# Kernel optimization log

Measured on AMD Instinct MI355X. Metric: run time of the kernel, lower is better.

Reference implementation:

```python
import jax, jax.numpy as jnp
import numpy as np

B, T, H, S, OBS, ACT = 64, 256, 1024, 128, 1024, 32


def setup_inputs() -> dict:
    key = jax.random.key(0)
    ks = jax.random.split(key, 9)
    w = lambda k, shape, fan_in: jax.random.normal(k, shape, jnp.float32) / np.sqrt(fan_in).astype(np.float32)
    return {
        "obs": jax.random.normal(ks[0], (B, T, OBS), jnp.float32),
        "action": jax.random.normal(ks[1], (B, T, ACT), jnp.float32),
        "resets": jnp.zeros((B,), jnp.bool_),
        "noise": jax.random.normal(ks[2], (B, T, S), jnp.float32),
        # GRUCell params (PyTorch layout: gates ordered r,z,n)
        "w_ih": w(ks[3], (3 * H, S + ACT), S + ACT),
        "w_hh": w(ks[4], (3 * H, H), H),
        "b_ih": jnp.zeros((3 * H,), jnp.float32),
        "b_hh": jnp.zeros((3 * H,), jnp.float32),
        # prior MLP: H -> H//2 -> 2S
        "pr_w1": w(ks[5], (H // 2, H), H),
        "pr_b1": jnp.zeros((H // 2,), jnp.float32),
        "pr_w2": w(ks[6], (2 * S, H // 2), H // 2),
        "pr_b2": jnp.zeros((2 * S,), jnp.float32),
        # posterior MLP: (H+OBS) -> (H+OBS)//2 -> 2S
        "po_w1": w(ks[7], ((H + OBS) // 2, H + OBS), H + OBS),
        "po_b1": jnp.zeros(((H + OBS) // 2,), jnp.float32),
        "po_w2": w(ks[8], (2 * S, (H + OBS) // 2), (H + OBS) // 2),
        "po_b2": jnp.zeros((2 * S,), jnp.float32),
    }


def reference(obs, action, resets, noise, w_ih, w_hh, b_ih, b_hh,
              pr_w1, pr_b1, pr_w2, pr_b2, po_w1, po_b1, po_w2, po_b2):
    Bv, Tv, _ = obs.shape
    keep = (~resets).astype(obs.dtype)[:, None]  # [B,1]; multiplies h,z for t>0
    # prev_action: zeros at t=0, action[:, t-1] afterwards
    prev_act = jnp.concatenate([jnp.zeros_like(action[:, :1]), action[:, :-1]], axis=1)

    def step(carry, xs):
        h, z = carry
        a_t, o_t, n_t, t_pos = xs
        m = jnp.where(t_pos > 0, keep, jnp.ones_like(keep))
        h = h * m
        z = z * m
        x = jnp.concatenate([z, a_t], axis=-1)
        gi = x @ w_ih.T + b_ih
        gh = h @ w_hh.T + b_hh
        ir, iz, inn = jnp.split(gi, 3, axis=-1)
        hr, hz, hn = jnp.split(gh, 3, axis=-1)
        r = jax.nn.sigmoid(ir + hr)
        u = jax.nn.sigmoid(iz + hz)
        n = jnp.tanh(inn + r * hn)
        h = (1.0 - u) * n + u * h
        pp = jax.nn.relu(h @ pr_w1.T + pr_b1) @ pr_w2.T + pr_b2
        pm, ps = jnp.split(pp, 2, axis=-1)
        ps = jax.nn.softplus(ps) + 1e-6
        qp = jax.nn.relu(jnp.concatenate([h, o_t], axis=-1) @ po_w1.T + po_b1) @ po_w2.T + po_b2
        qm, qs = jnp.split(qp, 2, axis=-1)
        qs = jax.nn.softplus(qs) + 1e-6
        z = qm + qs * n_t  # reparameterized rsample
        return (h, z), (h, z, pm, ps, qm, qs)

    h0 = jnp.zeros((Bv, w_hh.shape[-1]), obs.dtype)
    z0 = jnp.zeros((Bv, noise.shape[-1]), obs.dtype)
    xs = (jnp.swapaxes(prev_act, 0, 1), jnp.swapaxes(obs, 0, 1),
          jnp.swapaxes(noise, 0, 1), jnp.arange(Tv))
    _, (hs, zs, pm, ps, qm, qs) = jax.lax.scan(step, (h0, z0), xs)
    h_seq = jnp.swapaxes(hs, 0, 1)  # [B,T,H]
    z_seq = jnp.swapaxes(zs, 0, 1)  # [B,T,S]
    to_last = lambda a: jnp.moveaxis(a, 0, -1)  # torch stacks dists along dim=-1 -> [B,S,T]
    return (to_last(pm), to_last(ps), to_last(qm), to_last(qs), h_seq, z_seq)
```

## Files before the change

### kernel.cpp

```cpp
#include <hip/hip_runtime.h>

#define B_ 64
#define T_ 256
#define H_ 1024
#define S_ 128
#define OBS_ 1024
#define ACT_ 32

typedef __attribute__((ext_vector_type(8))) short bf16x8;
typedef __attribute__((ext_vector_type(4))) float f32x4;

#define MFMA(a, b, c) __builtin_amdgcn_mfma_f32_16x16x32_bf16((a), (b), (c), 0, 0, 0)

__device__ __forceinline__ float bf2f(short s) {
    unsigned int u = ((unsigned int)(unsigned short)s) << 16;
    float f; __builtin_memcpy(&f, &u, 4); return f;
}
__device__ __forceinline__ short f2bf(float f) {
    unsigned int u; __builtin_memcpy(&u, &f, 4);
    unsigned int r = (u + 0x7fffu + ((u >> 16) & 1u)) >> 16;
    return (short)r;
}
__device__ __forceinline__ bf16x8 ld8(const short* p) { return *(const bf16x8*)p; }
__device__ __forceinline__ bf16x8 cvt8(const float* p) {
    bf16x8 r;
#pragma unroll
    for (int i = 0; i < 8; ++i) r[i] = f2bf(p[i]);
    return r;
}
__device__ __forceinline__ bf16x8 lda8(const short* p) {
    const unsigned long long* q8 = (const unsigned long long*)p;
    union { unsigned long long q[2]; bf16x8 v; } u;
    u.q[0] = __hip_atomic_load(q8, __ATOMIC_RELAXED, __HIP_MEMORY_SCOPE_AGENT);
    u.q[1] = __hip_atomic_load(q8 + 1, __ATOMIC_RELAXED, __HIP_MEMORY_SCOPE_AGENT);
    return u.v;
}
__device__ __forceinline__ void sta8(short* p, unsigned long long v) {
    __hip_atomic_store((unsigned long long*)p, v, __ATOMIC_RELAXED, __HIP_MEMORY_SCOPE_AGENT);
}
__device__ __forceinline__ unsigned long long pk4(float4 v) {
    return (unsigned long long)(unsigned short)f2bf(v.x)
         | ((unsigned long long)(unsigned short)f2bf(v.y) << 16)
         | ((unsigned long long)(unsigned short)f2bf(v.z) << 32)
         | ((unsigned long long)(unsigned short)f2bf(v.w) << 48);
}
__device__ __forceinline__ float sigm(float x) { return 1.f / (1.f + __expf(-x)); }
__device__ __forceinline__ float tanh_f(float x) { return 1.f - 2.f / (__expf(2.f * x) + 1.f); }
__device__ __forceinline__ float splus(float x) { return (x > 20.f) ? x : log1pf(__expf(x)); }

__device__ __forceinline__ void gridbar(int* flags, int e) {
    __syncthreads();
    if (threadIdx.x == 0)
        __hip_atomic_store(&flags[blockIdx.x * 16], e, __ATOMIC_RELAXED, __HIP_MEMORY_SCOPE_AGENT);
    if (threadIdx.x < 64) {
        while (__hip_atomic_load(&flags[threadIdx.x * 16], __ATOMIC_RELAXED,
                                 __HIP_MEMORY_SCOPE_AGENT) < e)
            __builtin_amdgcn_s_sleep(1);
    }
    __syncthreads();
}

__global__ void f2bf_arr(const float* __restrict__ src, short* __restrict__ dst, int n4) {
    int i = blockIdx.x * blockDim.x + threadIdx.x;
    if (i < n4) {
        float4 v = ((const float4*)src)[i];
        short4 o;
        o.x = f2bf(v.x); o.y = f2bf(v.y); o.z = f2bf(v.z); o.w = f2bf(v.w);
        ((short4*)dst)[i] = o;
    }
}

__global__ __launch_bounds__(256) void obs_gemm(
    const float* __restrict__ obs, const short* __restrict__ po_w1,
    const float* __restrict__ po_b1, short* __restrict__ part) {
    const int t = blockIdx.x;
    const int rg = threadIdx.x >> 6, lane = threadIdx.x & 63;
    const int c = lane & 15, q = lane >> 4;
    bf16x8 afr[32];
    const float* ap = obs + ((size_t)(rg * 16 + c) * T_ + t) * OBS_;
#pragma unroll
    for (int kb = 0; kb < 32; ++kb) afr[kb] = cvt8(ap + kb * 32 + q * 8);
    for (int jt = 0; jt < 64; ++jt) {
        f32x4 acc = {0.f, 0.f, 0.f, 0.f};
        const short* wgt = po_w1 + (size_t)(jt * 16 + c) * 2048 + 1024;
#pragma unroll 8
        for (int kb = 0; kb < 32; ++kb) acc = MFMA(afr[kb], ld8(wgt + kb * 32 + q * 8), acc);
        const float bias = po_b1[jt * 16 + c];
#pragma unroll
        for (int e = 0; e < 4; ++e) {
            const int br = rg * 16 + q * 4 + e;
            part[((size_t)t * 64 + br) * 1024 + jt * 16 + c] = f2bf(acc[e] + bias);
        }
    }
}

__global__ __launch_bounds__(256, 1) void rssm_scan(
    const short* __restrict__ act_bf, const unsigned char* __restrict__ resets,
    const short* __restrict__ w_ih, const short* __restrict__ w_hh,
    const float* __restrict__ b_ih, const float* __restrict__ b_hh,
    const short* __restrict__ po_w1, const short* __restrict__ po_w2,
    const float* __restrict__ po_b2, const short* __restrict__ part,
    const float* __restrict__ noise,
    int* flags, short* h_bf, short* z_bf, short* poh,
    float* __restrict__ out_h, float* __restrict__ out_qm,
    float* __restrict__ out_qs, float* __restrict__ out_z) {
    extern __shared__ __align__(16) char smem[];
    bf16x8* wlds = (bf16x8*)smem;
    __shared__ __align__(16) float stg[64][20];
    const int tid = threadIdx.x, bid = blockIdx.x;
    const int rg = tid >> 6, lane = tid & 63, c = lane & 15, q = lane >> 4;
    const int j0 = bid * 16, m0 = rg * 16, arow = m0 + c, n = j0 + c;
    const int srow = tid >> 2, sseg = tid & 3;
    const bf16x8 zv8 = {0, 0, 0, 0, 0, 0, 0, 0};

    for (int i = 0; i < 32; ++i) {
        const int fid = i * 256 + tid;
        const int g = fid >> 11, kb = (fid >> 6) & 31, ln = fid & 63;
        const int cc = ln & 15, qq = ln >> 4;
        const short* src = (g == 0)
            ? po_w1 + (size_t)(j0 + cc) * 2048 + kb * 32 + qq * 8
            : w_hh + (size_t)((g - 1) * 1024 + j0 + cc) * 1024 + kb * 32 + qq * 8;
        wlds[fid] = ld8(src);
    }
    __syncthreads();

    const bool rsA = resets[arow] != 0;
    bool rsR[4];
#pragma unroll
    for (int e = 0; e < 4; ++e) rsR[e] = resets[m0 + q * 4 + e] != 0;
    const short* wiR = w_ih + (size_t)n * 160;
    const short* wiU = w_ih + (size_t)(1024 + n) * 160;
    const short* wiN = w_ih + (size_t)(2048 + n) * 160;
    const float biR = b_ih[n], bhR = b_hh[n];
    const float biU = b_ih[1024 + n], bhU = b_hh[1024 + n];
    const float biN = b_ih[2048 + n], bhN = b_hh[2048 + n];
    const short* ha = h_bf + arow * 1024;
    const bf16x8* wPl = wlds;
    const bf16x8* wRl = wlds + 2048;
    const bf16x8* wUl = wlds + 4096;
    const bf16x8* wNl = wlds + 6144;
    const int s2 = (bid < 8) ? j0 + c : 0;
    const short* wm = po_w2 + (size_t)s2 * 1024;
    const short* ws2 = po_w2 + (size_t)(128 + s2) * 1024;
    const float bM = (bid < 8) ? po_b2[s2] : 0.f;
    const float bS = (bid < 8) ? po_b2[128 + s2] : 0.f;

    f32x4 hp = {0.f, 0.f, 0.f, 0.f};
    f32x4 gR = {0.f, 0.f, 0.f, 0.f};
    f32x4 gU = {0.f, 0.f, 0.f, 0.f};
    f32x4 gN = {0.f, 0.f, 0.f, 0.f};
    f32x4 pinit;
#pragma unroll
    for (int e = 0; e < 4; ++e)
        pinit[e] = bf2f(part[((size_t)0 * 64 + m0 + q * 4 + e) * 1024 + n]);

    int ep = 1;
    for (int t = 0; t < T_; ++t) {
        f32x4 iR = {0.f, 0.f, 0.f, 0.f};
        f32x4 iU = iR, iN = iR;
        if (t > 0) {
            const short* za = z_bf + arow * 128;
#pragma unroll
            for (int kb = 0; kb < 4; ++kb) {
                const int k = kb * 32 + q * 8;
                bf16x8 a = rsA ? zv8 : lda8(za + k);
                iR = MFMA(a, ld8(wiR + k), iR);
                iU = MFMA(a, ld8(wiU + k), iU);
                iN = MFMA(a, ld8(wiN + k), iN);
            }
            const int k = q * 8;
            bf16x8 a2 = ld8(act_bf + (size_t)arow * (T_ * ACT_) + (size_t)(t - 1) * ACT_ + k);
            iR = MFMA(a2, ld8(wiR + 128 + k), iR);
            iU = MFMA(a2, ld8(wiU + 128 + k), iU);
            iN = MFMA(a2, ld8(wiN + 128 + k), iN);
        }
#pragma unroll
        for (int e = 0; e < 4; ++e) {
            const float hpv = (t > 0 && rsR[e]) ? 0.f : hp[e];
            const float r = sigm(iR[e] + gR[e] + biR + bhR);
            const float u = sigm(iU[e] + gU[e] + biU + bhU);
            const float nn = tanh_f(iN[e] + biN + r * (gN[e] + bhN));
            const float hv = (1.f - u) * nn + u * hpv;
            hp[e] = hv;
            stg[m0 + q * 4 + e][c] = hv;
        }
        __syncthreads();
        {
            float4 hv4 = *(const float4*)&stg[srow][sseg * 4];
            sta8(h_bf + srow * 1024 + j0 + sseg * 4, pk4(hv4));
            *(float4*)(out_h + (size_t)srow * (T_ * H_) + (size_t)t * H_ + j0 + sseg * 4) = hv4;
        }
        gridbar(flags, ep++);
        {
            f32x4 accP = pinit;
            f32x4 nR = {0.f, 0.f, 0.f, 0.f};
            f32x4 nU = nR, nN = nR;
#pragma unroll 8
            for (int kb = 0; kb < 32; ++kb) {
                const int k = kb * 32 + q * 8;
                bf16x8 a = lda8(ha + k);
                bf16x8 am = rsA ? zv8 : a;
                accP = MFMA(a, wPl[kb * 64 + lane], accP);
                nR = MFMA(am, wRl[kb * 64 + lane], nR);
                nU = MFMA(am, wUl[kb * 64 + lane], nU);
                nN = MFMA(am, wNl[kb * 64 + lane], nN);
            }
            gR = nR; gU = nU; gN = nN;
#pragma unroll
            for (int e = 0; e < 4; ++e) stg[m0 + q * 4 + e][c] = fmaxf(accP[e], 0.f);
        }
        if (t + 1 < T_) {
#pragma unroll
            for (int e = 0; e < 4; ++e)
                pinit[e] = bf2f(part[((size_t)(t + 1) * 64 + m0 + q * 4 + e) * 1024 + n]);
        }
        float nz[4];
        if (bid < 8) {
#pragma unroll
            for (int e = 0; e < 4; ++e)
                nz[e] = noise[(size_t)(m0 + q * 4 + e) * (T_ * S_) + (size_t)t * S_ + s2];
        }
        __syncthreads();
        {
            float4 v4 = *(const float4*)&stg[srow][sseg * 4];
            sta8(poh + srow * 1024 + j0 + sseg * 4, pk4(v4));
        }
        gridbar(flags, ep++);
        if (bid < 8) {
            f32x4 aM = {0.f, 0.f, 0.f, 0.f};
            f32x4 aS = aM;
            const short* pa = poh + arow * 1024;
#pragma unroll 8
            for (int kb = 0; kb < 32; ++kb) {
                const int k = kb * 32 + q * 8;
                bf16x8 a = lda8(pa + k);
                aM = MFMA(a, ld8(wm + k), aM);
                aS = MFMA(a, ld8(ws2 + k), aS);
            }
#pragma unroll
            for (int e = 0; e < 4; ++e) {
                const int row = m0 + q * 4 + e;
                const float qm = aM[e] + bM;
                const float qs = splus(aS[e] + bS) + 1e-6f;
                stg[row][c] = qm + qs * nz[e];
                out_qm[(size_t)row * (S_ * T_) + (size_t)s2 * T_ + t] = qm;
                out_qs[(size_t)row * (S_ * T_) + (size_t)s2 * T_ + t] = qs;
            }
            __syncthreads();
            {
                float4 z4 = *(const float4*)&stg[srow][sseg * 4];
                *(float4*)(out_z + (size_t)srow * (T_ * S_) + (size_t)t * S_ + j0 + sseg * 4) = z4;
                sta8(z_bf + srow * 128 + j0 + sseg * 4, pk4(z4));
            }
        }
        gridbar(flags, ep++);
    }
}

__global__ __launch_bounds__(256) void prior_mlp(
    const float* __restrict__ hseq, const short* __restrict__ pr_w1,
    const float* __restrict__ pr_b1, const short* __restrict__ pr_w2,
    const float* __restrict__ pr_b2, float* __restrict__ out_pm,
    float* __restrict__ out_ps) {
    __shared__ __align__(16) short hid[64][512];
    const int w = threadIdx.x >> 6;
    const int lane = threadIdx.x & 63;
    const int c = lane & 15, q = lane >> 4;
    const long rb0 = (long)blockIdx.x * 64;
    bf16x8 afr[32];
    const float* ap = hseq + (rb0 + w * 16 + c) * 1024;
#pragma unroll
    for (int kb = 0; kb < 32; ++kb) afr[kb] = cvt8(ap + kb * 32 + q * 8);
    for (int jt = 0; jt < 32; ++jt) {
        f32x4 acc = {0.f, 0.f, 0.f, 0.f};
        const short* wgt = pr_w1 + (size_t)(jt * 16 + c) * 1024;
#pragma unroll 8
        for (int kb = 0; kb < 32; ++kb) acc = MFMA(afr[kb], ld8(wgt + kb * 32 + q * 8), acc);
        const float bias = pr_b1[jt * 16 + c];
#pragma unroll
        for (int e = 0; e < 4; ++e)
            hid[w * 16 + q * 4 + e][jt * 16 + c] = f2bf(fmaxf(acc[e] + bias, 0.f));
    }
    __syncthreads();
    bf16x8 afr2[16];
#pragma unroll
    for (int kb = 0; kb < 16; ++kb) afr2[kb] = *(const bf16x8*)(&hid[w * 16 + c][kb * 32 + q * 8]);
    for (int jt = 0; jt < 16; ++jt) {
        f32x4 acc = {0.f, 0.f, 0.f, 0.f};
        const short* wgt = pr_w2 + (size_t)(jt * 16 + c) * 512;
#pragma unroll 8
        for (int kb = 0; kb < 16; ++kb) acc = MFMA(afr2[kb], ld8(wgt + kb * 32 + q * 8), acc);
        const int col = jt * 16 + c;
#pragma unroll
        for (int e = 0; e < 4; ++e) {
            const long rgidx = rb0 + w * 16 + q * 4 + e;
            const int b_ = (int)(rgidx >> 8), t_ = (int)(rgidx & 255);
            if (col < S_) {
                out_pm[(size_t)b_ * (S_ * T_) + (size_t)col * T_ + t_] = acc[e] + pr_b2[col];
            } else {
                out_ps[(size_t)b_ * (S_ * T_) + (size_t)(col - S_) * T_ + t_] =
                    splus(acc[e] + pr_b2[col]) + 1e-6f;
            }
        }
    }
}

extern "C" void kernel_launch(void* const* d_in, const int* in_sizes, int n_in,
                              void* d_out, int out_size, void* d_ws, size_t ws_size,
                              hipStream_t stream) {
    const float* obs = (const float*)d_in[0];
    const float* action = (const float*)d_in[1];
    const unsigned char* resets = (const unsigned char*)d_in[2];
    const float* noise = (const float*)d_in[3];
    const float* w_ih = (const float*)d_in[4];
    const float* w_hh = (const float*)d_in[5];
    const float* b_ih = (const float*)d_in[6];
    const float* b_hh = (const float*)d_in[7];
    const float* pr_w1 = (const float*)d_in[8];
    const float* pr_b1 = (const float*)d_in[9];
    const float* pr_w2 = (const float*)d_in[10];
    const float* pr_b2 = (const float*)d_in[11];
    const float* po_w1 = (const float*)d_in[12];
    const float* po_b1 = (const float*)d_in[13];
    const float* po_w2 = (const float*)d_in[14];
    const float* po_b2 = (const float*)d_in[15];

    float* out = (float*)d_out;
    const size_t BST = (size_t)B_ * S_ * T_;
    float* out_pm = out;
    float* out_ps = out + BST;
    float* out_qm = out + 2 * BST;
    float* out_qs = out + 3 * BST;
    float* out_h = out + 4 * BST;
    float* out_z = out + 4 * BST + (size_t)B_ * T_ * H_;

    char* w = (char*)d_ws;
    int* flags = (int*)w;
    short* h_bf = (short*)(w + 4096);
    short* z_bf = (short*)(w + 266240);
    short* poh = (short*)(w + 282624);
    short* act_bf = (short*)(w + 413696);
    short* w_ih_bf = (short*)(w + 1462272);
    short* w_hh_bf = (short*)(w + 2445312);
    short* po_w1_bf = (short*)(w + 8736768);
    short* po_w2_bf = (short*)(w + 12931072);
    short* pr_w1_bf = (short*)(w + 13455360);
    short* pr_w2_bf = (short*)(w + 14503936);
    short* part = (short*)(w + 14766080);

    static bool attr_set = false;
    if (!attr_set) {
        hipFuncSetAttribute(reinterpret_cast<const void*>(&rssm_scan),
                            hipFuncAttributeMaxDynamicSharedMemorySize, 131072);
        attr_set = true;
    }

    auto cvt = [&](const float* s, short* d, int n) {
        int n4 = n / 4;
        f2bf_arr<<<dim3((n4 + 255) / 256), 256, 0, stream>>>(s, d, n4);
    };
    cvt(action, act_bf, B_ * T_ * ACT_);
    cvt(w_ih, w_ih_bf, 3 * H_ * (S_ + ACT_));
    cvt(w_hh, w_hh_bf, 3 * H_ * H_);
    cvt(po_w1, po_w1_bf, 1024 * 2048);
    cvt(po_w2, po_w2_bf, 256 * 1024);
    cvt(pr_w1, pr_w1_bf, 512 * 1024);
    cvt(pr_w2, pr_w2_bf, 256 * 512);

    obs_gemm<<<dim3(256), 256, 0, stream>>>(obs, po_w1_bf, po_b1, part);

    rssm_scan<<<dim3(64), 256, 131072, stream>>>(
        act_bf, resets, w_ih_bf, w_hh_bf, b_ih, b_hh,
        po_w1_bf, po_w2_bf, po_b2, part, noise,
        flags, h_bf, z_bf, poh, out_h, out_qm, out_qs, out_z);

    prior_mlp<<<dim3(256), 256, 0, stream>>>(out_h, pr_w1_bf, pr_b1, pr_w2_bf, pr_b2,
                                             out_pm, out_ps);
}
```

Baseline: 9.624 ms.

## Batch-prefetch h/poh/z fragments with plain loads, stage w_ih in LDS

Result: slower. 11.93 ms (+24.0%).

```diff
diff --git a/kernel.cpp b/kernel.cpp
--- a/kernel.cpp
+++ b/kernel.cpp
@@ -27,13 +27,6 @@
 #pragma unroll
     for (int i = 0; i < 8; ++i) r[i] = f2bf(p[i]);
     return r;
-}
-__device__ __forceinline__ bf16x8 lda8(const short* p) {
-    const unsigned long long* q8 = (const unsigned long long*)p;
-    union { unsigned long long q[2]; bf16x8 v; } u;
-    u.q[0] = __hip_atomic_load(q8, __ATOMIC_RELAXED, __HIP_MEMORY_SCOPE_AGENT);
-    u.q[1] = __hip_atomic_load(q8 + 1, __ATOMIC_RELAXED, __HIP_MEMORY_SCOPE_AGENT);
-    return u.v;
 }
 __device__ __forceinline__ void sta8(short* p, unsigned long long v) {
     __hip_atomic_store((unsigned long long*)p, v, __ATOMIC_RELAXED, __HIP_MEMORY_SCOPE_AGENT);
@@ -57,6 +50,7 @@
                                  __HIP_MEMORY_SCOPE_AGENT) < e)
             __builtin_amdgcn_s_sleep(1);
     }
+    __builtin_amdgcn_fence(__ATOMIC_ACQUIRE, "agent");
     __syncthreads();
 }
 
@@ -122,15 +116,18 @@
             : w_hh + (size_t)((g - 1) * 1024 + j0 + cc) * 1024 + kb * 32 + qq * 8;
         wlds[fid] = ld8(src);
     }
+    bf16x8* wih = wlds + 8192;
+    for (int f = tid; f < 960; f += 256) {
+        const int g = f / 320, rem = f % 320, kk = rem >> 6, ln = rem & 63;
+        const int cc = ln & 15, qq = ln >> 4;
+        wih[f] = ld8(w_ih + (size_t)(g * 1024 + j0 + cc) * 160 + kk * 32 + qq * 8);
+    }
     __syncthreads();
 
     const bool rsA = resets[arow] != 0;
     bool rsR[4];
 #pragma unroll
     for (int e = 0; e < 4; ++e) rsR[e] = resets[m0 + q * 4 + e] != 0;
-    const short* wiR = w_ih + (size_t)n * 160;
-    const short* wiU = w_ih + (size_t)(1024 + n) * 160;
-    const short* wiN = w_ih + (size_t)(2048 + n) * 160;
     const float biR = b_ih[n], bhR = b_hh[n];
     const float biU = b_ih[1024 + n], bhU = b_hh[1024 + n];
     const float biN = b_ih[2048 + n], bhN = b_hh[2048 + n];
@@ -139,6 +136,9 @@
     const bf16x8* wRl = wlds + 2048;
     const bf16x8* wUl = wlds + 4096;
     const bf16x8* wNl = wlds + 6144;
+    const bf16x8* wiRl = wih;
+    const bf16x8* wiUl = wih + 320;
+    const bf16x8* wiNl = wih + 640;
     const int s2 = (bid < 8) ? j0 + c : 0;
     const short* wm = po_w2 + (size_t)s2 * 1024;
     const short* ws2 = po_w2 + (size_t)(128 + s2) * 1024;
@@ -160,19 +160,20 @@
         f32x4 iU = iR, iN = iR;
         if (t > 0) {
             const short* za = z_bf + arow * 128;
+            bf16x8 zfr[4];
+#pragma unroll
+            for (int kb = 0; kb < 4; ++kb) zfr[kb] = ld8(za + kb * 32 + q * 8);
+            bf16x8 a2 = ld8(act_bf + (size_t)arow * (T_ * ACT_) + (size_t)(t - 1) * ACT_ + q * 8);
 #pragma unroll
             for (int kb = 0; kb < 4; ++kb) {
-                const int k = kb * 32 + q * 8;
-                bf16x8 a = rsA ? zv8 : lda8(za + k);
-                iR = MFMA(a, ld8(wiR + k), iR);
-                iU = MFMA(a, ld8(wiU + k), iU);
-                iN = MFMA(a, ld8(wiN + k), iN);
-            }
-            const int k = q * 8;
-            bf16x8 a2 = ld8(act_bf + (size_t)arow * (T_ * ACT_) + (size_t)(t - 1) * ACT_ + k);
-            iR = MFMA(a2, ld8(wiR + 128 + k), iR);
-            iU = MFMA(a2, ld8(wiU + 128 + k), iU);
-            iN = MFMA(a2, ld8(wiN + 128 + k), iN);
+                bf16x8 a = rsA ? zv8 : zfr[kb];
+                iR = MFMA(a, wiRl[kb * 64 + lane], iR);
+                iU = MFMA(a, wiUl[kb * 64 + lane], iU);
+                iN = MFMA(a, wiNl[kb * 64 + lane], iN);
+            }
+            iR = MFMA(a2, wiRl[256 + lane], iR);
+            iU = MFMA(a2, wiUl[256 + lane], iU);
+            iN = MFMA(a2, wiNl[256 + lane], iN);
         }
 #pragma unroll
         for (int e = 0; e < 4; ++e) {
@@ -191,14 +192,27 @@
             *(float4*)(out_h + (size_t)srow * (T_ * H_) + (size_t)t * H_ + j0 + sseg * 4) = hv4;
         }
         gridbar(flags, ep++);
+        float nz[4];
         {
+            bf16x8 hfr[32];
+#pragma unroll
+            for (int kb = 0; kb < 32; ++kb) hfr[kb] = ld8(ha + kb * 32 + q * 8);
             f32x4 accP = pinit;
+            if (t + 1 < T_) {
+#pragma unroll
+                for (int e = 0; e < 4; ++e)
+                    pinit[e] = bf2f(part[((size_t)(t + 1) * 64 + m0 + q * 4 + e) * 1024 + n]);
+            }
+            if (bid < 8) {
+#pragma unroll
+                for (int e = 0; e < 4; ++e)
+                    nz[e] = noise[(size_t)(m0 + q * 4 + e) * (T_ * S_) + (size_t)t * S_ + s2];
+            }
             f32x4 nR = {0.f, 0.f, 0.f, 0.f};
             f32x4 nU = nR, nN = nR;
 #pragma unroll 8
             for (int kb = 0; kb < 32; ++kb) {
-                const int k = kb * 32 + q * 8;
-                bf16x8 a = lda8(ha + k);
+                bf16x8 a = hfr[kb];
                 bf16x8 am = rsA ? zv8 : a;
                 accP = MFMA(a, wPl[kb * 64 + lane], accP);
                 nR = MFMA(am, wRl[kb * 64 + lane], nR);
@@ -209,17 +223,6 @@
 #pragma unroll
             for (int e = 0; e < 4; ++e) stg[m0 + q * 4 + e][c] = fmaxf(accP[e], 0.f);
         }
-        if (t + 1 < T_) {
-#pragma unroll
-            for (int e = 0; e < 4; ++e)
-                pinit[e] = bf2f(part[((size_t)(t + 1) * 64 + m0 + q * 4 + e) * 1024 + n]);
-        }
-        float nz[4];
-        if (bid < 8) {
-#pragma unroll
-            for (int e = 0; e < 4; ++e)
-                nz[e] = noise[(size_t)(m0 + q * 4 + e) * (T_ * S_) + (size_t)t * S_ + s2];
-        }
         __syncthreads();
         {
             float4 v4 = *(const float4*)&stg[srow][sseg * 4];
@@ -227,15 +230,16 @@
         }
         gridbar(flags, ep++);
         if (bid < 8) {
+            bf16x8 pfr[32];
+            const short* pa = poh + arow * 1024;
+#pragma unroll
+            for (int kb = 0; kb < 32; ++kb) pfr[kb] = ld8(pa + kb * 32 + q * 8);
             f32x4 aM = {0.f, 0.f, 0.f, 0.f};
             f32x4 aS = aM;
-            const short* pa = poh + arow * 1024;
 #pragma unroll 8
             for (int kb = 0; kb < 32; ++kb) {
-                const int k = kb * 32 + q * 8;
-                bf16x8 a = lda8(pa + k);
-                aM = MFMA(a, ld8(wm + k), aM);
-                aS = MFMA(a, ld8(ws2 + k), aS);
+                aM = MFMA(pfr[kb], ld8(wm + kb * 32 + q * 8), aM);
+                aS = MFMA(pfr[kb], ld8(ws2 + kb * 32 + q * 8), aS);
             }
 #pragma unroll
             for (int e = 0; e < 4; ++e) {
@@ -351,7 +355,7 @@
     static bool attr_set = false;
     if (!attr_set) {
         hipFuncSetAttribute(reinterpret_cast<const void*>(&rssm_scan),
-                            hipFuncAttributeMaxDynamicSharedMemorySize, 131072);
+                            hipFuncAttributeMaxDynamicSharedMemorySize, 146432);
         attr_set = true;
     }
 
@@ -369,7 +373,7 @@
 
     obs_gemm<<<dim3(256), 256, 0, stream>>>(obs, po_w1_bf, po_b1, part);
 
-    rssm_scan<<<dim3(64), 256, 131072, stream>>>(
+    rssm_scan<<<dim3(64), 256, 146432, stream>>>(
         act_bf, resets, w_ih_bf, w_hh_bf, b_ih, b_hh,
         po_w1_bf, po_w2_bf, po_b2, part, noise,
         flags, h_bf, z_bf, poh, out_h, out_qm, out_qs, out_z);
```
